# Performance work log

Hardware: AMD Instinct MI355X
Metric: run time of the kernel (lower is better)

## Reference

```python
import jax, jax.numpy as jnp
import numpy as np


def _build_resonance(T):
    """res[i,j] = Omega(gcd(i+1, j+1)) = sum_p min(v_p(i+1), v_p(j+1))."""
    n = np.arange(1, T + 1)
    g = np.gcd.outer(n, n)  # [T,T], values in 1..T
    # smallest-prime-factor sieve up to T, then Omega (prime factors w/ multiplicity)
    spf = np.arange(T + 1)
    for i in range(2, int(T ** 0.5) + 1):
        if spf[i] == i:
            sl = spf[i * i:: i]
            np.minimum(sl, i, out=sl)
    omega = np.zeros(T + 1, np.int64)
    for m in range(2, T + 1):
        omega[m] = omega[m // spf[m]] + 1
    return omega[g].astype(np.float32)


def _build_buffers(T):
    res = _build_resonance(T)
    causal = np.tril(np.ones((T, T), np.float32))
    ident = np.eye(T, dtype=np.float32)
    allowed = ((res > 0) | (ident > 0)) & (causal > 0)  # bool [T,T]
    rbias = np.log1p(res) * allowed.astype(np.float32)
    return jnp.asarray(rbias), jnp.asarray(allowed)


def setup_inputs() -> dict:
    key = jax.random.key(0)
    B, T, C, H = 8, 2048, 1024, 64
    kx, kq, kk, kv = jax.random.split(key, 4)
    x = jax.random.normal(kx, (B, T, C), dtype=jnp.float32)
    scale = C ** -0.5
    Wq = jax.random.normal(kq, (C, H), dtype=jnp.float32) * scale
    Wk = jax.random.normal(kk, (C, H), dtype=jnp.float32) * scale
    Wv = jax.random.normal(kv, (C, H), dtype=jnp.float32) * scale
    rbias, allowed = _build_buffers(T)
    return {"x": x, "Wq": Wq, "Wk": Wk, "Wv": Wv, "rbias": rbias, "allowed": allowed}


def reference(x, Wq, Wk, Wv, rbias, allowed):
    B, T, C = x.shape
    q = x @ Wq  # [B,T,H]
    k = x @ Wk
    v = x @ Wv
    w = jnp.einsum("bth,bsh->bts", q, k) * (C ** -0.5)  # note: scaled by C, as in source
    w = w + rbias[:T, :T]
    w = jnp.where(allowed[:T, :T], w, -jnp.inf)
    a = jax.nn.softmax(w, axis=-1)  # every row has diagonal allowed -> no NaN
    return a @ v  # [B,T,H]
```

## Files before the change

kernel.cpp:

```cpp
#include <hip/hip_runtime.h>

#define T_SEQ 2048
#define NB    8
#define CDIM  1024
#define HDIM  64
#define PPB   80

typedef __attribute__((ext_vector_type(8))) short short8;
typedef __attribute__((ext_vector_type(4))) float float4v;

__device__ inline short f2bf(float x) {
    unsigned u = __builtin_bit_cast(unsigned int, x);
    u += 0x7FFFu + ((u >> 16) & 1u);
    return (short)(u >> 16);
}

__device__ inline void dma16(const void* g, void* l) {
    __builtin_amdgcn_global_load_lds(
        (const __attribute__((address_space(1))) unsigned int*)g,
        (__attribute__((address_space(3))) unsigned int*)l, 16, 0, 0);
}

__global__ __launch_bounds__(256) void wcvt_kernel(
    const float* __restrict__ Wq, const float* __restrict__ Wk,
    const float* __restrict__ Wv, short* __restrict__ Wbt)
{
    __shared__ float tile[64][65];
    const int w  = blockIdx.y;
    const int k0 = blockIdx.x * 64;
    const float* Ws[3] = {Wq, Wk, Wv};
    const float* W = Ws[w];
    const int n  = threadIdx.x & 63;
    const int kq = threadIdx.x >> 6;
#pragma unroll
    for (int i = 0; i < 16; ++i) {
        int kk = kq + i * 4;
        tile[kk][n] = W[(size_t)(k0 + kk) * HDIM + n];
    }
    __syncthreads();
    const int kk = threadIdx.x & 63;
#pragma unroll
    for (int i = 0; i < 16; ++i) {
        int nn = kq + i * 4;
        Wbt[((size_t)(w * HDIM + nn)) * CDIM + k0 + kk] = f2bf(tile[kk][nn]);
    }
}

__global__ __launch_bounds__(256) void proj_kernel(
    const float* __restrict__ x, const short* __restrict__ Wbt,
    short* __restrict__ qb, short* __restrict__ kb, short* __restrict__ vtb)
{
    __shared__ short As[2][32 * 64];
    __shared__ short Bs[2][192 * 64];

    const int tid  = threadIdx.x;
    const int wave = tid >> 6, lane = tid & 63;
    const int quad = lane >> 4, l16 = lane & 15;
    const int m0   = blockIdx.x * 32;
    const int arow = tid >> 3;
    const int ac8  = (tid & 7) * 8;

    const float* xsrc = x + (size_t)(m0 + arow) * CDIM + ac8;

    float4v acc[2][3];
#pragma unroll
    for (int mt = 0; mt < 2; ++mt)
#pragma unroll
        for (int i = 0; i < 3; ++i) acc[mt][i] = (float4v){0.f, 0.f, 0.f, 0.f};

    {
        float4 a0 = *(const float4*)(xsrc);
        float4 a1 = *(const float4*)(xsrc + 4);
#pragma unroll
        for (int i = 0; i < 6; ++i)
            dma16(Wbt + (size_t)(i * 32 + arow) * CDIM + ac8,
                  &Bs[0][i * 2048 + tid * 8]);
        short8 s;
        s[0] = f2bf(a0.x); s[1] = f2bf(a0.y); s[2] = f2bf(a0.z); s[3] = f2bf(a0.w);
        s[4] = f2bf(a1.x); s[5] = f2bf(a1.y); s[6] = f2bf(a1.z); s[7] = f2bf(a1.w);
        *(short8*)&As[0][arow * 64 + ac8] = s;
    }

    int p = 0;
    for (int kt = 0; kt < 16; ++kt) {
        __syncthreads();
        const bool more = (kt + 1) < 16;
        float4 a0, a1;
        if (more) {
            const float* src = xsrc + (kt + 1) * 64;
            a0 = *(const float4*)(src);
            a1 = *(const float4*)(src + 4);
#pragma unroll
            for (int i = 0; i < 6; ++i)
                dma16(Wbt + (size_t)(i * 32 + arow) * CDIM + (kt + 1) * 64 + ac8,
                      &Bs[p ^ 1][i * 2048 + tid * 8]);
        }
#pragma unroll
        for (int ks = 0; ks < 2; ++ks) {
            short8 af[2];
#pragma unroll
            for (int mt = 0; mt < 2; ++mt)
                af[mt] = *(const short8*)&As[p][(mt * 16 + l16) * 64 + ks * 32 + quad * 8];
#pragma unroll
            for (int i = 0; i < 3; ++i) {
                const int ct = wave * 3 + i;
                short8 bf_ = *(const short8*)&Bs[p][(ct * 16 + l16) * 64 + ks * 32 + quad * 8];
#pragma unroll
                for (int mt = 0; mt < 2; ++mt)
                    acc[mt][i] = __builtin_amdgcn_mfma_f32_16x16x32_bf16(af[mt], bf_, acc[mt][i], 0, 0, 0);
            }
        }
        if (more) {
            short8 s;
            s[0] = f2bf(a0.x); s[1] = f2bf(a0.y); s[2] = f2bf(a0.z); s[3] = f2bf(a0.w);
            s[4] = f2bf(a1.x); s[5] = f2bf(a1.y); s[6] = f2bf(a1.z); s[7] = f2bf(a1.w);
            *(short8*)&As[p ^ 1][arow * 64 + ac8] = s;
        }
        p ^= 1;
    }

#pragma unroll
    for (int i = 0; i < 3; ++i) {
        const int ctg = wave * 3 + i;
        const int mat = ctg >> 2;
        const int n   = (ctg & 3) * 16 + l16;
#pragma unroll
        for (int mt = 0; mt < 2; ++mt)
#pragma unroll
            for (int r = 0; r < 4; ++r) {
                const int m = m0 + mt * 16 + quad * 4 + r;
                if (mat == 0)      qb[(size_t)m * HDIM + n] = f2bf(acc[mt][i][r] * 0.03125f);
                else if (mat == 1) kb[(size_t)m * HDIM + n] = f2bf(acc[mt][i][r]);
                else {
                    int bb = m >> 11, tt = m & (T_SEQ - 1);
                    vtb[((size_t)bb * HDIM + n) * T_SEQ + tt] = f2bf(acc[mt][i][r]);
                }
            }
    }
}

__global__ __launch_bounds__(256) void attn_part_kernel(
    const short* __restrict__ qb, const short* __restrict__ kb,
    const short* __restrict__ vtb, const float* __restrict__ rbias,
    float* __restrict__ Op, float2* __restrict__ mlp)
{
    __shared__ short Ks[2][64 * 64];
    __shared__ short Vs[2][64 * 64];
    __shared__ short Ps[4][16][72];

    const int b   = blockIdx.y;
    const int tid = threadIdx.x;
    const int wave = tid >> 6, lane = tid & 63;
    const int quad = lane >> 4, l16 = lane & 15;
    const int srow = tid >> 3;
    const int sc8  = (tid & 7) * 8;

    int qt64 = 0, c = blockIdx.x, cum = 0;
    while (true) { int ch = (qt64 + 8) >> 3; if (c < ch) break; c -= ch; cum += ch; ++qt64; }
    const int j0 = c * 8;
    const int j1 = (j0 + 8 < qt64 + 1) ? j0 + 8 : qt64 + 1;
    const int qrow0 = qt64 * 64 + wave * 16;

    const short* qptr = qb + (size_t)(b * T_SEQ + qrow0 + l16) * HDIM;
    short8 qf0 = *(const short8*)(qptr + quad * 8);
    short8 qf1 = *(const short8*)(qptr + 32 + quad * 8);

    float4v oacc[4];
#pragma unroll
    for (int i = 0; i < 4; ++i) oacc[i] = (float4v){0.f, 0.f, 0.f, 0.f};
    float m_run[4] = {-1e30f, -1e30f, -1e30f, -1e30f};
    float l_run[4] = {0.f, 0.f, 0.f, 0.f};

    {
        const int s0 = j0 * 64;
#pragma unroll
        for (int i = 0; i < 2; ++i) {
            dma16(kb + (size_t)(b * T_SEQ + s0 + i * 32 + srow) * HDIM + sc8,
                  &Ks[0][i * 2048 + tid * 8]);
            dma16(vtb + (size_t)(b * HDIM + i * 32 + srow) * T_SEQ + s0 + sc8,
                  &Vs[0][i * 2048 + tid * 8]);
        }
    }

    int p = 0;
    for (int j = j0; j < j1; ++j) {
        __syncthreads();
        if (j + 1 < j1) {
            const int sn = (j + 1) * 64;
#pragma unroll
            for (int i = 0; i < 2; ++i) {
                dma16(kb + (size_t)(b * T_SEQ + sn + i * 32 + srow) * HDIM + sc8,
                      &Ks[p ^ 1][i * 2048 + tid * 8]);
                dma16(vtb + (size_t)(b * HDIM + i * 32 + srow) * T_SEQ + sn + sc8,
                      &Vs[p ^ 1][i * 2048 + tid * 8]);
            }
        }
        const int s0 = j * 64;

        float rbv[4][4];
#pragma unroll
        for (int nt = 0; nt < 4; ++nt) {
            int s_idx = s0 + nt * 16 + l16;
#pragma unroll
            for (int r = 0; r < 4; ++r)
                rbv[nt][r] = rbias[(size_t)(qrow0 + quad * 4 + r) * T_SEQ + s_idx];
        }

        float4v sa[4];
#pragma unroll
        for (int nt = 0; nt < 4; ++nt) {
            short8 kf0 = *(const short8*)&Ks[p][(nt * 16 + l16) * 64 + quad * 8];
            short8 kf1 = *(const short8*)&Ks[p][(nt * 16 + l16) * 64 + 32 + quad * 8];
            float4v a = {0.f, 0.f, 0.f, 0.f};
            a = __builtin_amdgcn_mfma_f32_16x16x32_bf16(qf0, kf0, a, 0, 0, 0);
            a = __builtin_amdgcn_mfma_f32_16x16x32_bf16(qf1, kf1, a, 0, 0, 0);
            sa[nt] = a;
        }

        float pm[4][4];
        float mt[4] = {-1e30f, -1e30f, -1e30f, -1e30f};
#pragma unroll
        for (int nt = 0; nt < 4; ++nt) {
            int s_idx = s0 + nt * 16 + l16;
#pragma unroll
            for (int r = 0; r < 4; ++r) {
                int t_idx = qrow0 + quad * 4 + r;
                float rb = rbv[nt][r];
                bool ok = (rb > 0.f) || ((t_idx == 0) && (s_idx == 0));
                float sv = ok ? (sa[nt][r] + rb) : -1e30f;
                pm[nt][r] = sv;
                mt[r] = fmaxf(mt[r], sv);
            }
        }
#pragma unroll
        for (int off = 1; off < 16; off <<= 1)
#pragma unroll
            for (int r = 0; r < 4; ++r)
                mt[r] = fmaxf(mt[r], __shfl_xor(mt[r], off, 64));
        float alpha[4];
#pragma unroll
        for (int r = 0; r < 4; ++r) {
            float mn = fmaxf(m_run[r], mt[r]);
            alpha[r] = __expf(m_run[r] - mn);
            m_run[r] = mn;
        }
        float rs[4] = {0.f, 0.f, 0.f, 0.f};
#pragma unroll
        for (int nt = 0; nt < 4; ++nt)
#pragma unroll
            for (int r = 0; r < 4; ++r) {
                float pv = (pm[nt][r] > -1e29f) ? __expf(pm[nt][r] - m_run[r]) : 0.f;
                pm[nt][r] = pv;
                rs[r] += pv;
            }
#pragma unroll
        for (int off = 1; off < 16; off <<= 1)
#pragma unroll
            for (int r = 0; r < 4; ++r)
                rs[r] += __shfl_xor(rs[r], off, 64);
#pragma unroll
        for (int r = 0; r < 4; ++r) {
            l_run[r] = l_run[r] * alpha[r] + rs[r];
            oacc[0][r] *= alpha[r]; oacc[1][r] *= alpha[r];
            oacc[2][r] *= alpha[r]; oacc[3][r] *= alpha[r];
        }

#pragma unroll
        for (int nt = 0; nt < 4; ++nt)
#pragma unroll
            for (int r = 0; r < 4; ++r)
                Ps[wave][quad * 4 + r][nt * 16 + l16] = f2bf(pm[nt][r]);

#pragma unroll
        for (int ks = 0; ks < 2; ++ks) {
            short8 pf = *(const short8*)&Ps[wave][l16][ks * 32 + quad * 8];
#pragma unroll
            for (int ht = 0; ht < 4; ++ht) {
                short8 vf = *(const short8*)&Vs[p][(ht * 16 + l16) * 64 + ks * 32 + quad * 8];
                oacc[ht] = __builtin_amdgcn_mfma_f32_16x16x32_bf16(pf, vf, oacc[ht], 0, 0, 0);
            }
        }
        p ^= 1;
    }

    const int pidx = b * PPB + cum + c;
    float* obase = Op + (size_t)pidx * 4096;
#pragma unroll
    for (int ht = 0; ht < 4; ++ht)
#pragma unroll
        for (int r = 0; r < 4; ++r)
            obase[(wave * 16 + quad * 4 + r) * 64 + ht * 16 + l16] = oacc[ht][r];
    if (l16 == 0)
#pragma unroll
        for (int r = 0; r < 4; ++r)
            mlp[(size_t)pidx * 64 + wave * 16 + quad * 4 + r] = make_float2(m_run[r], l_run[r]);
}

__global__ __launch_bounds__(256) void attn_merge_kernel(
    const float* __restrict__ Op, const float2* __restrict__ mlp,
    float* __restrict__ out)
{
    const int qt16 = blockIdx.x;
    const int b    = blockIdx.y;
    const int qt64 = qt16 >> 2;
    const int nch  = (qt64 + 8) >> 3;
    int cum = 0;
    for (int i = 0; i < qt64; ++i) cum += (i + 8) >> 3;
    const int pbase = b * PPB + cum;
    const int col = threadIdx.x & 63;
    const int rq  = threadIdx.x >> 6;

#pragma unroll
    for (int rr = 0; rr < 4; ++rr) {
        const int row  = rq * 4 + rr;
        const int prow = (qt16 & 3) * 16 + row;
        float2 ml[4];
        for (int cc = 0; cc < nch; ++cc)
            ml[cc] = mlp[(size_t)(pbase + cc) * 64 + prow];
        float M = -1e30f;
        for (int cc = 0; cc < nch; ++cc) M = fmaxf(M, ml[cc].x);
        float L = 0.f, O = 0.f;
        for (int cc = 0; cc < nch; ++cc) {
            float w = __expf(ml[cc].x - M);
            L += ml[cc].y * w;
            O += Op[(size_t)(pbase + cc) * 4096 + prow * 64 + col] * w;
        }
        out[((size_t)(b * T_SEQ) + qt16 * 16 + row) * HDIM + col] = O / L;
    }
}

extern "C" void kernel_launch(void* const* d_in, const int* in_sizes, int n_in,
                              void* d_out, int out_size, void* d_ws, size_t ws_size,
                              hipStream_t stream) {
    (void)in_sizes; (void)n_in; (void)out_size; (void)ws_size;
    const float* x     = (const float*)d_in[0];
    const float* Wq    = (const float*)d_in[1];
    const float* Wk    = (const float*)d_in[2];
    const float* Wv    = (const float*)d_in[3];
    const float* rbias = (const float*)d_in[4];
    float* out = (float*)d_out;

    char* wsb   = (char*)d_ws;
    short* qb   = (short*)(wsb);
    short* kb   = (short*)(wsb + (size_t)2 * 1024 * 1024);
    short* vtb  = (short*)(wsb + (size_t)4 * 1024 * 1024);
    short* Wbt  = (short*)(wsb + (size_t)6 * 1024 * 1024);
    float* Op   = (float*)(wsb + (size_t)7 * 1024 * 1024);
    float2* mlp = (float2*)(wsb + (size_t)18 * 1024 * 1024);

    wcvt_kernel<<<dim3(16, 3), 256, 0, stream>>>(Wq, Wk, Wv, Wbt);
    proj_kernel<<<dim3(512), 256, 0, stream>>>(x, Wbt, qb, kb, vtb);
    attn_part_kernel<<<dim3(PPB, NB), 256, 0, stream>>>(qb, kb, vtb, rbias, Op, mlp);
    attn_merge_kernel<<<dim3(128, NB), 256, 0, stream>>>(Op, mlp, out);
}
```

Measured before the change: 197.8 us.

## XOR-swizzle LDS tiles in projection and attention; vectorize merge kernel

The projection and attention kernels now permute the 16-byte chunk each thread fetches with an XOR of its row index, so the LDS tiles are stored swizzled. The fragment reads apply the matching XOR. This spreads the 16-row MFMA fragment reads across LDS banks instead of hitting the same banks on 128-byte-stride rows. Separately, the merge kernel computes the partition offset in closed form and uses float4 loads and stores with a fixed 4-way unrolled combine. That combine reads unused partition slots and masks them out by setting their max to a large negative value.

```diff
diff --git a/kernel.cpp b/kernel.cpp
--- a/kernel.cpp
+++ b/kernel.cpp
@@ -58,9 +58,10 @@
     const int quad = lane >> 4, l16 = lane & 15;
     const int m0   = blockIdx.x * 32;
     const int arow = tid >> 3;
-    const int ac8  = (tid & 7) * 8;
-
-    const float* xsrc = x + (size_t)(m0 + arow) * CDIM + ac8;
+    const int achk = tid & 7;
+    const int gchk = (achk ^ (arow & 7)) * 8;
+
+    const float* xsrc = x + (size_t)(m0 + arow) * CDIM + achk * 8;
 
     float4v acc[2][3];
 #pragma unroll
@@ -73,12 +74,12 @@
         float4 a1 = *(const float4*)(xsrc + 4);
 #pragma unroll
         for (int i = 0; i < 6; ++i)
-            dma16(Wbt + (size_t)(i * 32 + arow) * CDIM + ac8,
+            dma16(Wbt + (size_t)(i * 32 + arow) * CDIM + gchk,
                   &Bs[0][i * 2048 + tid * 8]);
         short8 s;
         s[0] = f2bf(a0.x); s[1] = f2bf(a0.y); s[2] = f2bf(a0.z); s[3] = f2bf(a0.w);
         s[4] = f2bf(a1.x); s[5] = f2bf(a1.y); s[6] = f2bf(a1.z); s[7] = f2bf(a1.w);
-        *(short8*)&As[0][arow * 64 + ac8] = s;
+        *(short8*)&As[0][arow * 64 + gchk] = s;
     }
 
     int p = 0;
@@ -92,7 +93,7 @@
             a1 = *(const float4*)(src + 4);
 #pragma unroll
             for (int i = 0; i < 6; ++i)
-                dma16(Wbt + (size_t)(i * 32 + arow) * CDIM + (kt + 1) * 64 + ac8,
+                dma16(Wbt + (size_t)(i * 32 + arow) * CDIM + (kt + 1) * 64 + gchk,
                       &Bs[p ^ 1][i * 2048 + tid * 8]);
         }
 #pragma unroll
@@ -100,11 +101,13 @@
             short8 af[2];
 #pragma unroll
             for (int mt = 0; mt < 2; ++mt)
-                af[mt] = *(const short8*)&As[p][(mt * 16 + l16) * 64 + ks * 32 + quad * 8];
+                af[mt] = *(const short8*)&As[p][(mt * 16 + l16) * 64
+                         + (((ks * 4 + quad) ^ (l16 & 7)) * 8)];
 #pragma unroll
             for (int i = 0; i < 3; ++i) {
                 const int ct = wave * 3 + i;
-                short8 bf_ = *(const short8*)&Bs[p][(ct * 16 + l16) * 64 + ks * 32 + quad * 8];
+                short8 bf_ = *(const short8*)&Bs[p][(ct * 16 + l16) * 64
+                             + (((ks * 4 + quad) ^ (l16 & 7)) * 8)];
 #pragma unroll
                 for (int mt = 0; mt < 2; ++mt)
                     acc[mt][i] = __builtin_amdgcn_mfma_f32_16x16x32_bf16(af[mt], bf_, acc[mt][i], 0, 0, 0);
@@ -114,7 +117,7 @@
             short8 s;
             s[0] = f2bf(a0.x); s[1] = f2bf(a0.y); s[2] = f2bf(a0.z); s[3] = f2bf(a0.w);
             s[4] = f2bf(a1.x); s[5] = f2bf(a1.y); s[6] = f2bf(a1.z); s[7] = f2bf(a1.w);
-            *(short8*)&As[p ^ 1][arow * 64 + ac8] = s;
+            *(short8*)&As[p ^ 1][arow * 64 + gchk] = s;
         }
         p ^= 1;
     }
@@ -153,7 +156,7 @@
     const int wave = tid >> 6, lane = tid & 63;
     const int quad = lane >> 4, l16 = lane & 15;
     const int srow = tid >> 3;
-    const int sc8  = (tid & 7) * 8;
+    const int gchk = ((tid & 7) ^ (srow & 7)) * 8;
 
     int qt64 = 0, c = blockIdx.x, cum = 0;
     while (true) { int ch = (qt64 + 8) >> 3; if (c < ch) break; c -= ch; cum += ch; ++qt64; }
@@ -175,9 +178,9 @@
         const int s0 = j0 * 64;
 #pragma unroll
         for (int i = 0; i < 2; ++i) {
-            dma16(kb + (size_t)(b * T_SEQ + s0 + i * 32 + srow) * HDIM + sc8,
+            dma16(kb + (size_t)(b * T_SEQ + s0 + i * 32 + srow) * HDIM + gchk,
                   &Ks[0][i * 2048 + tid * 8]);
-            dma16(vtb + (size_t)(b * HDIM + i * 32 + srow) * T_SEQ + s0 + sc8,
+            dma16(vtb + (size_t)(b * HDIM + i * 32 + srow) * T_SEQ + s0 + gchk,
                   &Vs[0][i * 2048 + tid * 8]);
         }
     }
@@ -189,9 +192,9 @@
             const int sn = (j + 1) * 64;
 #pragma unroll
             for (int i = 0; i < 2; ++i) {
-                dma16(kb + (size_t)(b * T_SEQ + sn + i * 32 + srow) * HDIM + sc8,
+                dma16(kb + (size_t)(b * T_SEQ + sn + i * 32 + srow) * HDIM + gchk,
                       &Ks[p ^ 1][i * 2048 + tid * 8]);
-                dma16(vtb + (size_t)(b * HDIM + i * 32 + srow) * T_SEQ + sn + sc8,
+                dma16(vtb + (size_t)(b * HDIM + i * 32 + srow) * T_SEQ + sn + gchk,
                       &Vs[p ^ 1][i * 2048 + tid * 8]);
             }
         }
@@ -209,8 +212,9 @@
         float4v sa[4];
 #pragma unroll
         for (int nt = 0; nt < 4; ++nt) {
-            short8 kf0 = *(const short8*)&Ks[p][(nt * 16 + l16) * 64 + quad * 8];
-            short8 kf1 = *(const short8*)&Ks[p][(nt * 16 + l16) * 64 + 32 + quad * 8];
+            const int rbase = (nt * 16 + l16) * 64;
+            short8 kf0 = *(const short8*)&Ks[p][rbase + ((quad ^ (l16 & 7)) * 8)];
+            short8 kf1 = *(const short8*)&Ks[p][rbase + (((4 + quad) ^ (l16 & 7)) * 8)];
             float4v a = {0.f, 0.f, 0.f, 0.f};
             a = __builtin_amdgcn_mfma_f32_16x16x32_bf16(qf0, kf0, a, 0, 0, 0);
             a = __builtin_amdgcn_mfma_f32_16x16x32_bf16(qf1, kf1, a, 0, 0, 0);
@@ -276,7 +280,8 @@
             short8 pf = *(const short8*)&Ps[wave][l16][ks * 32 + quad * 8];
 #pragma unroll
             for (int ht = 0; ht < 4; ++ht) {
-                short8 vf = *(const short8*)&Vs[p][(ht * 16 + l16) * 64 + ks * 32 + quad * 8];
+                short8 vf = *(const short8*)&Vs[p][(ht * 16 + l16) * 64
+                            + (((ks * 4 + quad) ^ (l16 & 7)) * 8)];
                 oacc[ht] = __builtin_amdgcn_mfma_f32_16x16x32_bf16(pf, vf, oacc[ht], 0, 0, 0);
             }
         }
@@ -304,29 +309,37 @@
     const int b    = blockIdx.y;
     const int qt64 = qt16 >> 2;
     const int nch  = (qt64 + 8) >> 3;
-    int cum = 0;
-    for (int i = 0; i < qt64; ++i) cum += (i + 8) >> 3;
+    const int g8   = qt64 >> 3, rem = qt64 & 7;
+    const int cum  = 4 * g8 * (g8 + 1) + rem * (g8 + 1);
     const int pbase = b * PPB + cum;
-    const int col = threadIdx.x & 63;
-    const int rq  = threadIdx.x >> 6;
-
-#pragma unroll
-    for (int rr = 0; rr < 4; ++rr) {
-        const int row  = rq * 4 + rr;
-        const int prow = (qt16 & 3) * 16 + row;
-        float2 ml[4];
-        for (int cc = 0; cc < nch; ++cc)
-            ml[cc] = mlp[(size_t)(pbase + cc) * 64 + prow];
-        float M = -1e30f;
-        for (int cc = 0; cc < nch; ++cc) M = fmaxf(M, ml[cc].x);
-        float L = 0.f, O = 0.f;
-        for (int cc = 0; cc < nch; ++cc) {
-            float w = __expf(ml[cc].x - M);
-            L += ml[cc].y * w;
-            O += Op[(size_t)(pbase + cc) * 4096 + prow * 64 + col] * w;
-        }
-        out[((size_t)(b * T_SEQ) + qt16 * 16 + row) * HDIM + col] = O / L;
-    }
+
+    const int row = threadIdx.x >> 4;
+    const int c4  = (threadIdx.x & 15) * 4;
+    const int prow = (qt16 & 3) * 16 + row;
+
+    float2 ml[4];
+    float4 o4[4];
+#pragma unroll
+    for (int cc = 0; cc < 4; ++cc) {
+        ml[cc] = mlp[(size_t)(pbase + cc) * 64 + prow];
+        o4[cc] = *(const float4*)&Op[(size_t)(pbase + cc) * 4096 + prow * 64 + c4];
+        if (cc >= nch) ml[cc].x = -1e30f;
+    }
+    float M = -1e30f;
+#pragma unroll
+    for (int cc = 0; cc < 4; ++cc) M = fmaxf(M, ml[cc].x);
+    float L = 0.f;
+    float4 O = make_float4(0.f, 0.f, 0.f, 0.f);
+#pragma unroll
+    for (int cc = 0; cc < 4; ++cc) {
+        float w = __expf(ml[cc].x - M);
+        L += ml[cc].y * w;
+        O.x += o4[cc].x * w; O.y += o4[cc].y * w;
+        O.z += o4[cc].z * w; O.w += o4[cc].w * w;
+    }
+    float inv = 1.0f / L;
+    float4 res = make_float4(O.x * inv, O.y * inv, O.z * inv, O.w * inv);
+    *(float4*)&out[((size_t)(b * T_SEQ) + qt16 * 16 + row) * HDIM + c4] = res;
 }
 
 extern "C" void kernel_launch(void* const* d_in, const int* in_sizes, int n_in,
```

Result: faster. 172.0 us (-13.0%).
